# Optimization experiments

Measured on AMD Instinct MI355X. Metric: run time of the kernel, lower is better.

Reference implementation:

```python
import jax, jax.numpy as jnp
import numpy as np

N_SAMPLES = 32768  # exp.n_samples = 2**15
N_EVENTS = 16      # VectorwiseSparsity keep=16
HOP = 256          # start = indices[b, i] * 256


def setup_inputs() -> dict:
    key = jax.random.key(0)
    k1, k2 = jax.random.split(key)
    # synthesized per-event audio (batch, n_events, n_samples)
    x = jax.random.normal(k1, (128, N_EVENTS, N_SAMPLES), dtype=jnp.float32)
    # frame indices from the sparsity module; start offsets are indices*256,
    # and start + n_samples must fit in the 2*n_samples buffer -> idx < 128
    indices = jax.random.randint(k2, (128, N_EVENTS), 0, N_SAMPLES // HOP, dtype=jnp.int64)
    return {"x": x, "indices": indices}


def reference(x, indices):
    # Faithful, vectorized form of:
    #   output = zeros(B, 1, 2*N)
    #   for b, i: output[b, :, idx[b,i]*256 : idx[b,i]*256 + N] += x[b, i]
    #   output = output[..., :N]
    B, E, N = x.shape
    buf = jnp.zeros((B, 2 * N), dtype=x.dtype)
    # absolute sample positions for every event sample: (B, E, N)
    pos = indices[:, :, None] * HOP + jnp.arange(N)
    b_idx = jnp.arange(B)[:, None, None]
    buf = buf.at[b_idx, pos].add(x)  # overlap-add scatter
    return buf[:, None, :N]  # (B, 1, N)
```

## Files before the change

### kernel.cpp

```cpp
#include <hip/hip_runtime.h>

#define N_SAMPLES 32768
#define N_EVENTS 16
#define HOP 256
#define TILE 1024

__global__ __launch_bounds__(256) void ola_gather_kernel(
    const float* __restrict__ x,
    const int* __restrict__ indices,
    float* __restrict__ out)
{
    const int tile = blockIdx.x & 31;
    const int b    = blockIdx.x >> 5;
    const int s0   = tile * TILE + threadIdx.x * 4;

    const float* xb = x + (size_t)b * N_EVENTS * N_SAMPLES;
    const int*   ib = indices + b * N_EVENTS;

    float4 acc = make_float4(0.f, 0.f, 0.f, 0.f);

#pragma unroll
    for (int i = 0; i < N_EVENTS; ++i) {
        const int start = ib[i] * HOP;
        if (s0 >= start) {
            const float4 v = *reinterpret_cast<const float4*>(
                xb + (size_t)i * N_SAMPLES + (s0 - start));
            acc.x += v.x; acc.y += v.y; acc.z += v.z; acc.w += v.w;
        }
    }

    *reinterpret_cast<float4*>(out + (size_t)b * N_SAMPLES + s0) = acc;
}

extern "C" void kernel_launch(void* const* d_in, const int* in_sizes, int n_in,
                              void* d_out, int out_size, void* d_ws, size_t ws_size,
                              hipStream_t stream) {
    const float* x       = (const float*)d_in[0];
    const int*   indices = (const int*)d_in[1];
    float*       out     = (float*)d_out;

    const int blocks = 128 * (N_SAMPLES / TILE);
    ola_gather_kernel<<<blocks, 256, 0, stream>>>(x, indices, out);
}
```

Measured before the change: 30.11 us.

## Pair mirrored tiles per block for load balance and use nontemporal loads/stores

Each block now handles two tiles, p and 31-p, so tiles with few active events are paired with tiles that have many, which evens out work across blocks. The grid is halved to 2048 blocks and reordered so the batch index varies fastest. Loads and stores use nontemporal builtins so the data read once does not pollute the cache. The risks are fewer blocks in flight and higher register use per thread.

```diff
diff --git a/kernel.cpp b/kernel.cpp
--- a/kernel.cpp
+++ b/kernel.cpp
@@ -5,31 +5,41 @@
 #define HOP 256
 #define TILE 1024
 
+typedef float f32x4 __attribute__((ext_vector_type(4)));
+
 __global__ __launch_bounds__(256) void ola_gather_kernel(
     const float* __restrict__ x,
     const int* __restrict__ indices,
     float* __restrict__ out)
 {
-    const int tile = blockIdx.x & 31;
-    const int b    = blockIdx.x >> 5;
-    const int s0   = tile * TILE + threadIdx.x * 4;
+    const int p  = blockIdx.x >> 7;
+    const int b  = blockIdx.x & 127;
+    const int sA = p * TILE + threadIdx.x * 4;
+    const int sB = (31 - p) * TILE + threadIdx.x * 4;
 
     const float* xb = x + (size_t)b * N_EVENTS * N_SAMPLES;
     const int*   ib = indices + b * N_EVENTS;
 
-    float4 acc = make_float4(0.f, 0.f, 0.f, 0.f);
+    f32x4 accA = (f32x4)0.f;
+    f32x4 accB = (f32x4)0.f;
 
 #pragma unroll
     for (int i = 0; i < N_EVENTS; ++i) {
         const int start = ib[i] * HOP;
-        if (s0 >= start) {
-            const float4 v = *reinterpret_cast<const float4*>(
-                xb + (size_t)i * N_SAMPLES + (s0 - start));
-            acc.x += v.x; acc.y += v.y; acc.z += v.z; acc.w += v.w;
+        const float* row = xb + (size_t)i * N_SAMPLES;
+        if (sA >= start) {
+            accA += __builtin_nontemporal_load(
+                reinterpret_cast<const f32x4*>(row + (sA - start)));
+        }
+        if (sB >= start) {
+            accB += __builtin_nontemporal_load(
+                reinterpret_cast<const f32x4*>(row + (sB - start)));
         }
     }
 
-    *reinterpret_cast<float4*>(out + (size_t)b * N_SAMPLES + s0) = acc;
+    float* ob = out + (size_t)b * N_SAMPLES;
+    __builtin_nontemporal_store(accA, reinterpret_cast<f32x4*>(ob + sA));
+    __builtin_nontemporal_store(accB, reinterpret_cast<f32x4*>(ob + sB));
 }
 
 extern "C" void kernel_launch(void* const* d_in, const int* in_sizes, int n_in,
@@ -39,6 +49,5 @@
     const int*   indices = (const int*)d_in[1];
     float*       out     = (float*)d_out;
 
-    const int blocks = 128 * (N_SAMPLES / TILE);
-    ola_gather_kernel<<<blocks, 256, 0, stream>>>(x, indices, out);
+    ola_gather_kernel<<<2048, 256, 0, stream>>>(x, indices, out);
 }
```

After: 30.02 us. About the same (-0.3%).
